# Kernel tuning notes

Hardware: AMD Instinct MI355X
Metric: run time of the kernel (lower is better)

## Reference

```python
import jax, jax.numpy as jnp
import numpy as np

XI = 10.0
LAMBDA_SCALE = 1e-4
NUM_CLASSES = 13
KNOWN_NUM_CLASSES = 12  # all labels except 'unknown'
EPS = 1e-10
B, D = 262144, 512


def setup_inputs() -> dict:
    key = jax.random.key(0)
    k1, k2, k3, k4, k5 = jax.random.split(key, 5)
    logits = jax.random.normal(k1, (B, NUM_CLASSES), dtype=jnp.float32)
    true_y = jax.random.randint(k2, (B,), 0, NUM_CLASSES, dtype=jnp.int64)
    is_unknown = jax.random.randint(k3, (B,), 0, 2, dtype=jnp.int32).astype(bool)
    deep_features = jax.random.normal(k4, (B, D), dtype=jnp.float32)
    weights = jax.random.uniform(k5, (NUM_CLASSES,), dtype=jnp.float32, minval=0.5, maxval=2.0)
    return {"logits": logits, "true_y": true_y, "is_unknown": is_unknown,
            "deep_features": deep_features, "weights": weights}


def reference(logits, true_y, is_unknown, deep_features, weights):
    # softmax over classes, then log(softmax + eps) as in the original
    sm = jax.nn.softmax(logits, axis=1)                      # [B, C]
    log_sm = jnp.log(sm + EPS)                               # [B, C]
    feat_mag = jnp.linalg.norm(deep_features, axis=1)        # [B]

    # unknown branch: uniform log-loss over all classes + squared-magnitude penalty
    je_unknown = -(1.0 / KNOWN_NUM_CLASSES) * jnp.sum(log_sm, axis=1)
    pen_unknown = feat_mag ** 2
    jr_unknown = je_unknown + LAMBDA_SCALE * pen_unknown

    # known branch: NLL of true class + hinge-squared magnitude penalty
    je_known = -jnp.take_along_axis(log_sm, true_y[:, None], axis=1)[:, 0]
    pen_known = jnp.maximum(XI - feat_mag, 0.0) ** 2
    jr_known = je_known + LAMBDA_SCALE * pen_known

    jr = jnp.where(is_unknown, jr_unknown, jr_known)         # [B]
    w = weights[true_y]                                      # [B]
    loss = jnp.sum(w * jr) / jnp.sum(w)
    return loss
```

## Files before the change

### kernel.cpp

```cpp
#include <hip/hip_runtime.h>
#include <math.h>


constexpr int CLS = 13;
constexpr int DF4 = 512 / 4;
constexpr float INV_KNOWN = 1.0f / 12.0f;
constexpr float LAM = 1e-4f;
constexpr float XI = 10.0f;

__global__ __launch_bounds__(256) void obj_main(
    const float*  __restrict__ logits,
    const int*    __restrict__ true_y,
    const int*    __restrict__ is_unknown,
    const float4* __restrict__ feat,
    const float*  __restrict__ weights,
    double*       __restrict__ partials,
    int B)
{
    const int lane = threadIdx.x & 63;
    const int wid  = threadIdx.x >> 6;
    const int nw   = blockDim.x >> 6;
    const int gw   = blockIdx.x * nw + wid;
    const int tw   = gridDim.x * nw;

    double num = 0.0, den = 0.0;

    int row = gw;
    float4 a, b;
    float  x = 0.0f;
    if (row < B) {
        const float4* fr = feat + (size_t)row * DF4;
        a = fr[lane];
        b = fr[lane + 64];
        if (lane < CLS) x = logits[(size_t)row * CLS + lane];
    }

    while (row < B) {
        const int nrow = row + tw;
        float4 na, nb;
        float  nx = 0.0f;
        if (nrow < B) {
            const float4* fr = feat + (size_t)nrow * DF4;
            na = fr[lane];
            nb = fr[lane + 64];
            if (lane < CLS) nx = logits[(size_t)nrow * CLS + lane];
        }

        float ss = fmaf(a.x, a.x, fmaf(a.y, a.y, fmaf(a.z, a.z, a.w * a.w)))
                 + fmaf(b.x, b.x, fmaf(b.y, b.y, fmaf(b.z, b.z, b.w * b.w)));
        float e  = (lane < CLS) ? __expf(x) : 0.0f;
        float S  = e;
        float sx = x;

        #pragma unroll
        for (int o = 32; o; o >>= 1) {
            ss += __shfl_xor(ss, o, 64);
            S  += __shfl_xor(S,  o, 64);
            sx += __shfl_xor(sx, o, 64);
        }

        const int   ty    = true_y[row];
        const int   unk   = is_unknown[row];
        const float logS  = __logf(S);
        const float x_ty  = __shfl(x, ty, 64);
        const float mag   = sqrtf(ss);

        const float jr_u = fmaf(LAM, ss, -INV_KNOWN * (sx - (float)CLS * logS));
        const float dk   = fmaxf(XI - mag, 0.0f);
        const float jr_k = fmaf(LAM, dk * dk, logS - x_ty);
        const float jr   = unk ? jr_u : jr_k;
        const float w    = weights[ty];

        num += (double)(w * jr);
        den += (double)w;

        row = nrow; a = na; b = nb; x = nx;
    }

    __shared__ double s_num[8], s_den[8];
    if (lane == 0) { s_num[wid] = num; s_den[wid] = den; }
    __syncthreads();
    if (threadIdx.x == 0) {
        double n = 0.0, d = 0.0;
        for (int i = 0; i < nw; ++i) { n += s_num[i]; d += s_den[i]; }
        partials[blockIdx.x] = n;
        partials[gridDim.x + blockIdx.x] = d;
    }
}

__global__ __launch_bounds__(256) void obj_final(
    const double* __restrict__ partials, int nparts, float* __restrict__ out)
{
    const int lane = threadIdx.x & 63;
    const int wid  = threadIdx.x >> 6;
    double n = 0.0, d = 0.0;
    for (int i = threadIdx.x; i < nparts; i += blockDim.x) {
        n += partials[i];
        d += partials[nparts + i];
    }
    #pragma unroll
    for (int o = 32; o; o >>= 1) {
        n += __shfl_xor(n, o, 64);
        d += __shfl_xor(d, o, 64);
    }
    __shared__ double s_n[4], s_d[4];
    if (lane == 0) { s_n[wid] = n; s_d[wid] = d; }
    __syncthreads();
    if (threadIdx.x == 0) {
        double tn = 0.0, td = 0.0;
        for (int i = 0; i < 4; ++i) { tn += s_n[i]; td += s_d[i]; }
        out[0] = (float)(tn / td);
    }
}

extern "C" void kernel_launch(void* const* d_in, const int* in_sizes, int n_in,
                              void* d_out, int out_size, void* d_ws, size_t ws_size,
                              hipStream_t stream)
{
    const float*  logits     = (const float*)d_in[0];
    const int*    true_y     = (const int*)d_in[1];
    const int*    is_unknown = (const int*)d_in[2];
    const float4* feat       = (const float4*)d_in[3];
    const float*  weights    = (const float*)d_in[4];
    float*        out        = (float*)d_out;
    const int B = in_sizes[1];

    double* partials = (double*)d_ws;
    constexpr int GRID = 2048, BLOCK = 256;

    obj_main<<<GRID, BLOCK, 0, stream>>>(logits, true_y, is_unknown, feat,
                                         weights, partials, B);
    obj_final<<<1, 256, 0, stream>>>(partials, GRID, out);
}
```

Measured before the change: 103.3 us.

## Tile rows per warp, stage logits in LDS, fuse final reduction via atomic counter

```diff
diff --git a/kernel.cpp b/kernel.cpp
--- a/kernel.cpp
+++ b/kernel.cpp
@@ -2,114 +2,143 @@
 #include <math.h>
 
 
-constexpr int CLS = 13;
-constexpr int DF4 = 512 / 4;
+typedef float f32x4 __attribute__((ext_vector_type(4)));
+constexpr int   CLS  = 13;
 constexpr float INV_KNOWN = 1.0f / 12.0f;
-constexpr float LAM = 1e-4f;
-constexpr float XI = 10.0f;
+constexpr float LAM  = 1e-4f;
+constexpr float XI   = 10.0f;
 
-__global__ __launch_bounds__(256) void obj_main(
+constexpr int RPW   = 32;
+constexpr int BLOCK = 256;
+constexpr int WPB   = BLOCK / 64;
+constexpr size_t COUNTER_OFF = 1u << 20;
+
+__global__ __launch_bounds__(256, 8) void obj_main(
     const float*  __restrict__ logits,
     const int*    __restrict__ true_y,
     const int*    __restrict__ is_unknown,
-    const float4* __restrict__ feat,
+    const f32x4*  __restrict__ feat,
     const float*  __restrict__ weights,
     double*       __restrict__ partials,
+    unsigned*     __restrict__ counter,
+    float*        __restrict__ out,
     int B)
 {
     const int lane = threadIdx.x & 63;
     const int wid  = threadIdx.x >> 6;
-    const int nw   = blockDim.x >> 6;
-    const int gw   = blockIdx.x * nw + wid;
-    const int tw   = gridDim.x * nw;
+    const int gw   = blockIdx.x * WPB + wid;
+    const int base_row = gw * RPW;
+
+    __shared__ float s_log[WPB][512];
+
+    {
+        const size_t lbase = (size_t)base_row * CLS;
+        const size_t ltot  = (size_t)B * CLS;
+        size_t i0 = lbase + (size_t)lane * 4;
+        size_t i1 = i0 + 256;
+        f32x4 v0 = (f32x4)0.0f, v1 = (f32x4)0.0f;
+        if (i0 + 4 <= ltot) v0 = *reinterpret_cast<const f32x4*>(logits + i0);
+        if (i1 + 4 <= ltot) v1 = *reinterpret_cast<const f32x4*>(logits + i1);
+        *reinterpret_cast<f32x4*>(&s_log[wid][lane * 4])       = v0;
+        *reinterpret_cast<f32x4*>(&s_log[wid][256 + lane * 4]) = v1;
+    }
+    int r_ld = base_row + (lane & 31); if (r_ld >= B) r_ld = B - 1;
+    const int   tyv  = true_y[r_ld];
+    const int   unkv = is_unknown[r_ld];
+    const float wv   = weights[lane < CLS ? lane : 0];
+    __syncthreads();
 
     double num = 0.0, den = 0.0;
-
-    int row = gw;
-    float4 a, b;
-    float  x = 0.0f;
+    int row = base_row;
+    f32x4 a = (f32x4)0.0f, b = (f32x4)0.0f;
     if (row < B) {
-        const float4* fr = feat + (size_t)row * DF4;
-        a = fr[lane];
-        b = fr[lane + 64];
-        if (lane < CLS) x = logits[(size_t)row * CLS + lane];
+        const f32x4* fr = feat + (size_t)row * 128;
+        a = __builtin_nontemporal_load(fr + lane);
+        b = __builtin_nontemporal_load(fr + lane + 64);
     }
 
-    while (row < B) {
-        const int nrow = row + tw;
-        float4 na, nb;
-        float  nx = 0.0f;
-        if (nrow < B) {
-            const float4* fr = feat + (size_t)nrow * DF4;
-            na = fr[lane];
-            nb = fr[lane + 64];
-            if (lane < CLS) nx = logits[(size_t)nrow * CLS + lane];
+    for (int rl = 0; rl < RPW && row < B; ++rl) {
+        f32x4 na = (f32x4)0.0f, nb = (f32x4)0.0f;
+        const int nrow = row + 1;
+        if (rl + 1 < RPW && nrow < B) {
+            const f32x4* fr = feat + (size_t)nrow * 128;
+            na = __builtin_nontemporal_load(fr + lane);
+            nb = __builtin_nontemporal_load(fr + lane + 64);
         }
 
         float ss = fmaf(a.x, a.x, fmaf(a.y, a.y, fmaf(a.z, a.z, a.w * a.w)))
                  + fmaf(b.x, b.x, fmaf(b.y, b.y, fmaf(b.z, b.z, b.w * b.w)));
-        float e  = (lane < CLS) ? __expf(x) : 0.0f;
-        float S  = e;
-        float sx = x;
+
+        const float x = (lane < CLS) ? s_log[wid][rl * CLS + lane] : 0.0f;
+        const float e = (lane < CLS) ? __expf(x) : 0.0f;
+        float S = e, sx = x;
 
         #pragma unroll
-        for (int o = 32; o; o >>= 1) {
-            ss += __shfl_xor(ss, o, 64);
+        for (int o = 32; o; o >>= 1) ss += __shfl_xor(ss, o, 64);
+        #pragma unroll
+        for (int o = 8; o; o >>= 1) {
             S  += __shfl_xor(S,  o, 64);
             sx += __shfl_xor(sx, o, 64);
         }
 
-        const int   ty    = true_y[row];
-        const int   unk   = is_unknown[row];
-        const float logS  = __logf(S);
-        const float x_ty  = __shfl(x, ty, 64);
-        const float mag   = sqrtf(ss);
+        const int   ty   = __shfl(tyv,  rl, 64);
+        const int   unk  = __shfl(unkv, rl, 64);
+        const float w    = __shfl(wv,   ty, 64);
+        const float x_ty = __shfl(x,    ty, 64);
+        const float logS = __logf(S);
+        const float mag  = sqrtf(ss);
 
         const float jr_u = fmaf(LAM, ss, -INV_KNOWN * (sx - (float)CLS * logS));
         const float dk   = fmaxf(XI - mag, 0.0f);
         const float jr_k = fmaf(LAM, dk * dk, logS - x_ty);
         const float jr   = unk ? jr_u : jr_k;
-        const float w    = weights[ty];
 
         num += (double)(w * jr);
         den += (double)w;
 
-        row = nrow; a = na; b = nb; x = nx;
+        row = nrow; a = na; b = nb;
     }
 
-    __shared__ double s_num[8], s_den[8];
-    if (lane == 0) { s_num[wid] = num; s_den[wid] = den; }
+    __shared__ double s_n[WPB], s_d[WPB];
+    __shared__ unsigned s_last;
+    if (lane == 0) { s_n[wid] = num; s_d[wid] = den; }
     __syncthreads();
     if (threadIdx.x == 0) {
         double n = 0.0, d = 0.0;
-        for (int i = 0; i < nw; ++i) { n += s_num[i]; d += s_den[i]; }
-        partials[blockIdx.x] = n;
-        partials[gridDim.x + blockIdx.x] = d;
+        for (int i = 0; i < WPB; ++i) { n += s_n[i]; d += s_d[i]; }
+        __hip_atomic_store(&partials[blockIdx.x], n,
+                           __ATOMIC_RELAXED, __HIP_MEMORY_SCOPE_AGENT);
+        __hip_atomic_store(&partials[gridDim.x + blockIdx.x], d,
+                           __ATOMIC_RELAXED, __HIP_MEMORY_SCOPE_AGENT);
+        __threadfence();
+        unsigned old = __hip_atomic_fetch_add(counter, 1u,
+                           __ATOMIC_ACQ_REL, __HIP_MEMORY_SCOPE_AGENT);
+        s_last = (old == gridDim.x - 1) ? 1u : 0u;
     }
-}
+    __syncthreads();
 
-__global__ __launch_bounds__(256) void obj_final(
-    const double* __restrict__ partials, int nparts, float* __restrict__ out)
-{
-    const int lane = threadIdx.x & 63;
-    const int wid  = threadIdx.x >> 6;
-    double n = 0.0, d = 0.0;
-    for (int i = threadIdx.x; i < nparts; i += blockDim.x) {
-        n += partials[i];
-        d += partials[nparts + i];
-    }
-    #pragma unroll
-    for (int o = 32; o; o >>= 1) {
-        n += __shfl_xor(n, o, 64);
-        d += __shfl_xor(d, o, 64);
-    }
-    __shared__ double s_n[4], s_d[4];
-    if (lane == 0) { s_n[wid] = n; s_d[wid] = d; }
-    __syncthreads();
-    if (threadIdx.x == 0) {
-        double tn = 0.0, td = 0.0;
-        for (int i = 0; i < 4; ++i) { tn += s_n[i]; td += s_d[i]; }
-        out[0] = (float)(tn / td);
+    if (s_last) {
+        __threadfence();
+        double n = 0.0, d = 0.0;
+        for (int i = threadIdx.x; i < (int)gridDim.x; i += blockDim.x) {
+            n += __hip_atomic_load(&partials[i],
+                     __ATOMIC_RELAXED, __HIP_MEMORY_SCOPE_AGENT);
+            d += __hip_atomic_load(&partials[gridDim.x + i],
+                     __ATOMIC_RELAXED, __HIP_MEMORY_SCOPE_AGENT);
+        }
+        #pragma unroll
+        for (int o = 32; o; o >>= 1) {
+            n += __shfl_xor(n, o, 64);
+            d += __shfl_xor(d, o, 64);
+        }
+        double* s_fd = (double*)&s_log[0][0];
+        if (lane == 0) { s_fd[wid] = n; s_fd[WPB + wid] = d; }
+        __syncthreads();
+        if (threadIdx.x == 0) {
+            double tn = 0.0, td = 0.0;
+            for (int i = 0; i < WPB; ++i) { tn += s_fd[i]; td += s_fd[WPB + i]; }
+            out[0] = (float)(tn / td);
+        }
     }
 }
 
@@ -120,15 +149,16 @@
     const float*  logits     = (const float*)d_in[0];
     const int*    true_y     = (const int*)d_in[1];
     const int*    is_unknown = (const int*)d_in[2];
-    const float4* feat       = (const float4*)d_in[3];
+    const f32x4*  feat       = (const f32x4*)d_in[3];
     const float*  weights    = (const float*)d_in[4];
     float*        out        = (float*)d_out;
     const int B = in_sizes[1];
 
-    double* partials = (double*)d_ws;
-    constexpr int GRID = 2048, BLOCK = 256;
+    const int grid = (B + WPB * RPW - 1) / (WPB * RPW);
+    double*   partials = (double*)d_ws;
+    unsigned* counter  = (unsigned*)((char*)d_ws + COUNTER_OFF);
 
-    obj_main<<<GRID, BLOCK, 0, stream>>>(logits, true_y, is_unknown, feat,
-                                         weights, partials, B);
-    obj_final<<<1, 256, 0, stream>>>(partials, GRID, out);
+    (void)hipMemsetAsync(counter, 0, sizeof(unsigned), stream);
+    obj_main<<<grid, BLOCK, 0, stream>>>(logits, true_y, is_unknown, feat,
+                                         weights, partials, counter, out, B);
 }
```

Result: slower. 276.9 us (+168.1%).
